# Optimization experiments

Hardware: AMD Instinct MI355X
Metric: run time of the kernel (lower is better)

## Reference

```python
import jax, jax.numpy as jnp
import numpy as np

N_USERS = 100000
N_ITEMS = 100000
N = N_USERS + N_ITEMS
E = 3200000
TXT = 768
GREC = 16
D = 32            # embedding_dim (hardcoded 32 in the torch module)
LAYERS = 3        # len(weight_size)


def setup_inputs() -> dict:
    key = jax.random.key(0)
    ks = jax.random.split(key, 20)
    inp = {}
    inp["edge_row"] = jax.random.randint(ks[0], (E,), 0, N, dtype=jnp.int32)
    inp["edge_col"] = jax.random.randint(ks[1], (E,), 0, N, dtype=jnp.int32)
    # normalized adjacency values (positive, small)
    inp["adj_vals"] = jax.random.uniform(ks[2], (E,), dtype=jnp.float32) * 0.1
    inp["user_name_embs"] = jax.random.normal(ks[3], (N_USERS, TXT), dtype=jnp.float32)
    inp["sent_embs"] = jax.random.normal(ks[4], (N_ITEMS, TXT), dtype=jnp.float32)
    # learned params
    inp["user_emb"] = jax.random.normal(ks[5], (N_USERS, GREC), dtype=jnp.float32) * 0.1
    inp["item_emb"] = jax.random.normal(ks[6], (N_ITEMS, GREC), dtype=jnp.float32) * 0.1
    inp["ue_W1"] = jax.random.normal(ks[7], (TXT, 32), dtype=jnp.float32) * 0.05
    inp["ue_W2"] = jax.random.normal(ks[8], (32, GREC), dtype=jnp.float32) * 0.05
    inp["ie_W1"] = jax.random.normal(ks[9], (TXT, 32), dtype=jnp.float32) * 0.05
    inp["ie_W2"] = jax.random.normal(ks[10], (32, GREC), dtype=jnp.float32) * 0.05
    inp["gc_W"] = jax.random.normal(ks[11], (LAYERS, D, D), dtype=jnp.float32) * 0.1
    inp["gc_b"] = jnp.zeros((LAYERS, D), dtype=jnp.float32)
    inp["bi_W"] = jax.random.normal(ks[12], (LAYERS, D, D), dtype=jnp.float32) * 0.1
    inp["bi_b"] = jnp.zeros((LAYERS, D), dtype=jnp.float32)
    return inp


def _ngcf_forward(edge_row, edge_col, adj_vals, user_name_embs, sent_embs,
                  user_emb, item_emb, ue_W1, ue_W2, ie_W1, ie_W2,
                  gc_W, gc_b, bi_W, bi_b):
    # text encoders (Dropout is identity in eval mode)
    u_created = jax.nn.relu(user_name_embs @ ue_W1) @ ue_W2   # [Nu, 16]
    i_created = jax.nn.relu(sent_embs @ ie_W1) @ ie_W2         # [Ni, 16]
    agg_user = jnp.concatenate([user_emb, u_created], axis=1)  # [Nu, 32]
    agg_item = jnp.concatenate([item_emb, i_created], axis=1)  # [Ni, 32]
    ego = jnp.concatenate([agg_user, agg_item], axis=0)        # [N, 32]

    all_embeddings = [ego]
    for l in range(LAYERS):
        # sparse.mm(adj, ego): gather source rows, scale by edge value, scatter-add
        gathered = adj_vals[:, None] * ego[edge_col]           # [E, 32]
        side = jax.ops.segment_sum(gathered, edge_row, num_segments=N)  # [N, 32]
        sum_emb = jax.nn.leaky_relu(side @ gc_W[l] + gc_b[l])
        bi_emb = jax.nn.leaky_relu((ego * side) @ bi_W[l] + bi_b[l])
        ego = sum_emb + bi_emb                                 # dropout = identity (eval)
        norm = ego / jnp.maximum(
            jnp.linalg.norm(ego, axis=1, keepdims=True), 1e-12)
        all_embeddings.append(norm)
    return jnp.concatenate(all_embeddings, axis=1)             # [N, 32*(LAYERS+1)]


def reference(edge_row, edge_col, adj_vals, user_name_embs, sent_embs,
              user_emb, item_emb, ue_W1, ue_W2, ie_W1, ie_W2,
              gc_W, gc_b, bi_W, bi_b):
    all_e = _ngcf_forward(edge_row, edge_col, adj_vals, user_name_embs, sent_embs,
                          user_emb, item_emb, ue_W1, ue_W2, ie_W1, ie_W2,
                          gc_W, gc_b, bi_W, bi_b)
    u_g = all_e[:N_USERS]
    i_g = all_e[N_USERS:]
    return (u_g, i_g)
```

## Files before the change

kernel.cpp:

```cpp
#include <hip/hip_runtime.h>
#include <cstdint>

#define NU 100000
#define NI 100000
#define NN 200000
#define NE 3200000
#define TXT 768
#define NBF 640

typedef _Float16 f16x8 __attribute__((ext_vector_type(8)));
typedef _Float16 f16x4 __attribute__((ext_vector_type(4)));
typedef float    f32x4 __attribute__((ext_vector_type(4)));

typedef __attribute__((address_space(1))) const unsigned int guint;
typedef __attribute__((address_space(3))) unsigned int luint;

__device__ __forceinline__ float lrelu(float x) { return x >= 0.f ? x : 0.01f * x; }

#define MEMFENCE asm volatile("" ::: "memory")
#define WAIT_VM(N)  asm volatile("s_waitcnt vmcnt(" #N ")" ::: "memory")
#define WAIT_LGKM0  asm volatile("s_waitcnt lgkmcnt(0)" ::: "memory")
#define BARRIER     do { __builtin_amdgcn_s_barrier(); MEMFENCE; } while (0)

__global__ __launch_bounds__(256) void prep_kernel(
    const int* __restrict__ erow,
    const float* __restrict__ uemb, const float* __restrict__ iemb,
    const float* __restrict__ ueW1, const float* __restrict__ ieW1,
    int* __restrict__ cnt,
    _Float16* __restrict__ ego16, float* __restrict__ outp,
    _Float16* __restrict__ w1p)
{
    const int b = blockIdx.x;
    const int tid = threadIdx.x;

    if (b < NBF) {
        const int4* e4 = (const int4*)erow;
        for (int c = b * 256 + tid; c < NE / 4; c += NBF * 256) {
            int4 v = e4[c];
            atomicAdd(&cnt[v.x], 1);
            atomicAdd(&cnt[v.y], 1);
            atomicAdd(&cnt[v.z], 1);
            atomicAdd(&cnt[v.w], 1);
        }
    } else if (b < NBF + 3125) {
        int idx = (b - NBF) * 256 + tid;
        if (idx >= NN * 4) return;
        int n = idx >> 2, q = idx & 3;
        float4 v;
        if (n < NU) v = ((const float4*)uemb)[(size_t)n * 4 + q];
        else        v = ((const float4*)iemb)[(size_t)(n - NU) * 4 + q];
        f16x4 h;
        h[0] = (_Float16)v.x; h[1] = (_Float16)v.y;
        h[2] = (_Float16)v.z; h[3] = (_Float16)v.w;
        *(f16x4*)(ego16 + (size_t)n * 32 + q * 4) = h;
        ((float4*)outp)[(size_t)n * 32 + q] = v;
    } else {
        int i = (b - (NBF + 3125)) * 256 + tid;
        int side = (i >= 24576);
        int ii = i - side * 24576;
        const float* W1 = side ? ieW1 : ueW1;
        int j   = ii & 7;
        int ln  = (ii >> 3) & 63;
        int kbH = ii >> 9;
        int kb  = kbH >> 1, H = kbH & 1;
        int k   = kb * 32 + (ln >> 4) * 8 + j;
        int c   = H * 16 + (ln & 15);
        w1p[i] = (_Float16)W1[k * 32 + c];
    }
}

__global__ __launch_bounds__(256) void scan_blk_kernel(const int* __restrict__ cnt,
                                                       int* __restrict__ rp,
                                                       int* __restrict__ bsum)
{
    __shared__ int ts[256];
    const int tid = threadIdx.x;
    const int base = blockIdx.x * 1024 + tid * 4;
    int v0 = (base + 0 < NN) ? cnt[base + 0] : 0;
    int v1 = (base + 1 < NN) ? cnt[base + 1] : 0;
    int v2 = (base + 2 < NN) ? cnt[base + 2] : 0;
    int v3 = (base + 3 < NN) ? cnt[base + 3] : 0;
    int s = v0 + v1 + v2 + v3;
    ts[tid] = s;
    __syncthreads();
    for (int off = 1; off < 256; off <<= 1) {
        int t = (tid >= off) ? ts[tid - off] : 0;
        __syncthreads();
        ts[tid] += t;
        __syncthreads();
    }
    int excl = ts[tid] - s;
    if (base + 0 < NN) rp[base + 0] = excl;
    if (base + 1 < NN) rp[base + 1] = excl + v0;
    if (base + 2 < NN) rp[base + 2] = excl + v0 + v1;
    if (base + 3 < NN) rp[base + 3] = excl + v0 + v1 + v2;
    if (tid == 255) bsum[blockIdx.x] = ts[255];
}

__global__ __launch_bounds__(256) void scan_bsum_kernel(int* __restrict__ bsum, int nblk)
{
    __shared__ int ts[256];
    const int tid = threadIdx.x;
    int v = (tid < nblk) ? bsum[tid] : 0;
    ts[tid] = v;
    __syncthreads();
    for (int off = 1; off < 256; off <<= 1) {
        int t = (tid >= off) ? ts[tid - off] : 0;
        __syncthreads();
        ts[tid] += t;
        __syncthreads();
    }
    if (tid < nblk) bsum[tid] = ts[tid] - v;
}

__global__ __launch_bounds__(256) void add_off_kernel(int* __restrict__ rp,
                                                      const int* __restrict__ bsum,
                                                      int* __restrict__ cur)
{
    int i = blockIdx.x * 256 + threadIdx.x;
    if (i < NN) {
        int v = rp[i] + bsum[i >> 10];
        rp[i] = v;
        cur[i] = v;
    }
    if (i == 0) rp[NN] = NE;
}

__global__ __launch_bounds__(256, 4) void mlp_fill_kernel(
    const float* __restrict__ Xu, const float* __restrict__ Xi,
    const _Float16* __restrict__ w1pack,
    const float* __restrict__ ueW2, const float* __restrict__ ieW2,
    _Float16* __restrict__ ego16,
    float* __restrict__ outp,
    const int* __restrict__ erow, const int* __restrict__ ecol,
    const float* __restrict__ eval,
    int* __restrict__ cur, uint2* __restrict__ recs)
{
    __shared__ float buf[2][4096];
    __shared__ float part[3][512];
    __shared__ _Float16 hbuf[640];

    const int tid = threadIdx.x;

    if (blockIdx.x >= 1024) {
        const int b = blockIdx.x - 1024;
        const int4*   e4 = (const int4*)erow;
        const int4*   c4 = (const int4*)ecol;
        const float4* f4 = (const float4*)eval;
        for (int c = b * 256 + tid; c < NE / 4; c += NBF * 256) {
            int4 v   = e4[c];
            int4 cc  = c4[c];
            float4 vv = f4[c];
            int p0 = atomicAdd(&cur[v.x], 1);
            recs[p0] = make_uint2((unsigned)cc.x | ((unsigned)(v.x & 63) << 18),
                                  __float_as_uint(vv.x));
            int p1 = atomicAdd(&cur[v.y], 1);
            recs[p1] = make_uint2((unsigned)cc.y | ((unsigned)(v.y & 63) << 18),
                                  __float_as_uint(vv.y));
            int p2 = atomicAdd(&cur[v.z], 1);
            recs[p2] = make_uint2((unsigned)cc.z | ((unsigned)(v.z & 63) << 18),
                                  __float_as_uint(vv.z));
            int p3 = atomicAdd(&cur[v.w], 1);
            recs[p3] = make_uint2((unsigned)cc.w | ((unsigned)(v.w & 63) << 18),
                                  __float_as_uint(vv.w));
        }
        return;
    }

    const int lane  = tid & 63;
    const int wv    = tid >> 6;
    const int row16 = lane & 15;
    const int cg    = lane >> 4;
    const int rx7   = row16 & 7;

    f16x8 bw2u, bw2i;
    #pragma unroll
    for (int j = 0; j < 8; ++j) {
        bw2u[j] = (_Float16)ueW2[((lane >> 4) * 8 + j) * 16 + (lane & 15)];
        bw2i[j] = (_Float16)ieW2[((lane >> 4) * 8 + j) * 16 + (lane & 15)];
    }

    const int tA = (int)(((long)blockIdx.x * 12500) >> 10);
    const int tB = (int)(((long)(blockIdx.x + 1) * 12500) >> 10);

    for (int t = tA; t < tB; ++t) {
        const bool isU = t < 6250;
        const int tile = isU ? t : t - 6250;
        const float* xt = (isU ? Xu : Xi) + (size_t)tile * 16 * TXT;
        const _Float16* w1p = w1pack + (isU ? 0 : 24576);

#define STAGE(bb, cc) do {                                                      \
            _Pragma("unroll")                                                   \
            for (int i_ = 0; i_ < 4; ++i_) {                                    \
                const int r_ = wv * 4 + i_;                                     \
                const float* g_ = xt + (size_t)r_ * TXT + (cc) * 256            \
                                  + ((lane ^ (r_ & 7)) << 2);                   \
                __builtin_amdgcn_global_load_lds((guint*)g_,                    \
                    (luint*)&buf[bb][r_ * 256], 16, 0, 0);                      \
            }                                                                   \
        } while (0)

#define MCHUNK(bb, cc) do {                                                     \
            _Pragma("unroll")                                                   \
            for (int kl2 = 0; kl2 < 2; ++kl2) {                                 \
                const int kbl = wv * 2 + kl2;                                   \
                const int kb  = (cc) * 8 + kbl;                                 \
                f16x8 b0 = *(const f16x8*)&w1p[(kb * 2 + 0) * 512 + lane * 8];  \
                f16x8 b1 = *(const f16x8*)&w1p[(kb * 2 + 1) * 512 + lane * 8];  \
                const int u0 = kbl * 8 + cg * 2;                                \
                f32x4 xa = *(const f32x4*)&buf[bb][row16 * 256 + ((u0 ^ rx7) << 2)]; \
                f32x4 xb = *(const f32x4*)&buf[bb][row16 * 256 + (((u0 + 1) ^ rx7) << 2)]; \
                f16x8 a;                                                        \
                a[0] = (_Float16)xa[0]; a[1] = (_Float16)xa[1];                 \
                a[2] = (_Float16)xa[2]; a[3] = (_Float16)xa[3];                 \
                a[4] = (_Float16)xb[0]; a[5] = (_Float16)xb[1];                 \
                a[6] = (_Float16)xb[2]; a[7] = (_Float16)xb[3];                 \
                c0 = __builtin_amdgcn_mfma_f32_16x16x32_f16(a, b0, c0, 0, 0, 0); \
                c1 = __builtin_amdgcn_mfma_f32_16x16x32_f16(a, b1, c1, 0, 0, 0); \
            }                                                                   \
        } while (0)

        f32x4 c0 = {0.f, 0.f, 0.f, 0.f};
        f32x4 c1 = {0.f, 0.f, 0.f, 0.f};

        STAGE(0, 0);
        STAGE(1, 1);
        WAIT_VM(4);
        BARRIER;
        MCHUNK(0, 0);
        WAIT_LGKM0;
        BARRIER;
        STAGE(0, 2);
        WAIT_VM(4);
        BARRIER;
        MCHUNK(1, 1);
        WAIT_LGKM0;
        WAIT_VM(0);
        BARRIER;
        MCHUNK(0, 2);
        WAIT_LGKM0;

        if (wv > 0) {
            *(f32x4*)&part[wv - 1][lane * 8]     = c0;
            *(f32x4*)&part[wv - 1][lane * 8 + 4] = c1;
            WAIT_LGKM0;
        }
        BARRIER;

        if (wv == 0) {
            #pragma unroll
            for (int p = 0; p < 3; ++p) {
                f32x4 pa = *(const f32x4*)&part[p][lane * 8];
                f32x4 pb = *(const f32x4*)&part[p][lane * 8 + 4];
                c0 += pa; c1 += pb;
            }
            #pragma unroll
            for (int j = 0; j < 4; ++j) {
                int r = cg * 4 + j;
                hbuf[r * 40 + row16]      = (_Float16)fmaxf(c0[j], 0.f);
                hbuf[r * 40 + row16 + 16] = (_Float16)fmaxf(c1[j], 0.f);
            }
            const _Float16* ap = &hbuf[row16 * 40 + cg * 8];
            f16x4 lo = *(const f16x4*)ap;
            f16x4 hi = *(const f16x4*)(ap + 4);
            f16x8 a2;
            a2[0] = lo[0]; a2[1] = lo[1]; a2[2] = lo[2]; a2[3] = lo[3];
            a2[4] = hi[0]; a2[5] = hi[1]; a2[6] = hi[2]; a2[7] = hi[3];

            f32x4 c2 = {0.f, 0.f, 0.f, 0.f};
            f16x8 bw2 = isU ? bw2u : bw2i;
            c2 = __builtin_amdgcn_mfma_f32_16x16x32_f16(a2, bw2, c2, 0, 0, 0);

            const int rbase = (isU ? 0 : NU) + tile * 16 + cg * 4;
            #pragma unroll
            for (int j = 0; j < 4; ++j) {
                float v = c2[j];
                ego16[(size_t)(rbase + j) * 32  + 16 + row16] = (_Float16)v;
                outp [(size_t)(rbase + j) * 128 + 16 + row16] = v;
            }
        }
#undef STAGE
#undef MCHUNK
    }
}

__global__ __launch_bounds__(256) void pull_update_v2(
    const int* __restrict__ rp, const uint2* __restrict__ recs,
    const _Float16* __restrict__ egoIn, _Float16* __restrict__ egoOut,
    float* __restrict__ outp,
    const float* __restrict__ gcW, const float* __restrict__ gcb,
    const float* __restrict__ biW, const float* __restrict__ bib, int l)
{
    __shared__ float acc[64][33];
    __shared__ float Wg[32][36];
    __shared__ float Wb[32][36];
    __shared__ float bgs[32], bbs[32];

    const int tid = threadIdx.x;
    for (int i = tid; i < 64 * 33; i += 256) ((float*)acc)[i] = 0.f;
    for (int i = tid; i < 1024; i += 256) {
        Wg[i >> 5][i & 31] = gcW[l * 1024 + i];
        Wb[i >> 5][i & 31] = biW[l * 1024 + i];
    }
    if (tid < 32) { bgs[tid] = gcb[l * 32 + tid]; bbs[tid] = bib[l * 32 + tid]; }

    const int r0 = blockIdx.x * 64;
    const int eBeg = rp[r0], eEnd = rp[r0 + 64];
    __syncthreads();

    const int cnt = eEnd - eBeg;
    const int s   = tid >> 3;
    const int q   = tid & 7;
    const int L   = (cnt + 31) >> 5;
    const int e0  = eBeg + s * L;
    const int e1  = min(e0 + L, eEnd);

    float4 a4 = make_float4(0.f, 0.f, 0.f, 0.f);
    int curRl = -1;

    auto PROC = [&](uint2 rr, f16x4 vv) {
        int rl = rr.x >> 18;
        float a = __uint_as_float(rr.y);
        if (rl != curRl) {
            if (curRl >= 0) {
                atomicAdd(&acc[curRl][q * 4 + 0], a4.x);
                atomicAdd(&acc[curRl][q * 4 + 1], a4.y);
                atomicAdd(&acc[curRl][q * 4 + 2], a4.z);
                atomicAdd(&acc[curRl][q * 4 + 3], a4.w);
            }
            a4 = make_float4(0.f, 0.f, 0.f, 0.f);
            curRl = rl;
        }
        a4.x += a * (float)vv[0];
        a4.y += a * (float)vv[1];
        a4.z += a * (float)vv[2];
        a4.w += a * (float)vv[3];
    };

    int e = e0;
    for (; e + 8 <= e1; e += 8) {
        uint2 r0r = recs[e],     r1r = recs[e + 1];
        uint2 r2r = recs[e + 2], r3r = recs[e + 3];
        uint2 r4r = recs[e + 4], r5r = recs[e + 5];
        uint2 r6r = recs[e + 6], r7r = recs[e + 7];
        f16x4 v0 = *(const f16x4*)(egoIn + (size_t)(r0r.x & 0x3FFFF) * 32 + q * 4);
        f16x4 v1 = *(const f16x4*)(egoIn + (size_t)(r1r.x & 0x3FFFF) * 32 + q * 4);
        f16x4 v2 = *(const f16x4*)(egoIn + (size_t)(r2r.x & 0x3FFFF) * 32 + q * 4);
        f16x4 v3 = *(const f16x4*)(egoIn + (size_t)(r3r.x & 0x3FFFF) * 32 + q * 4);
        f16x4 v4 = *(const f16x4*)(egoIn + (size_t)(r4r.x & 0x3FFFF) * 32 + q * 4);
        f16x4 v5 = *(const f16x4*)(egoIn + (size_t)(r5r.x & 0x3FFFF) * 32 + q * 4);
        f16x4 v6 = *(const f16x4*)(egoIn + (size_t)(r6r.x & 0x3FFFF) * 32 + q * 4);
        f16x4 v7 = *(const f16x4*)(egoIn + (size_t)(r7r.x & 0x3FFFF) * 32 + q * 4);
        PROC(r0r, v0); PROC(r1r, v1); PROC(r2r, v2); PROC(r3r, v3);
        PROC(r4r, v4); PROC(r5r, v5); PROC(r6r, v6); PROC(r7r, v7);
    }
    for (; e < e1; ++e) {
        uint2 rr = recs[e];
        f16x4 vv = *(const f16x4*)(egoIn + (size_t)(rr.x & 0x3FFFF) * 32 + q * 4);
        PROC(rr, vv);
    }
    if (curRl >= 0) {
        atomicAdd(&acc[curRl][q * 4 + 0], a4.x);
        atomicAdd(&acc[curRl][q * 4 + 1], a4.y);
        atomicAdd(&acc[curRl][q * 4 + 2], a4.z);
        atomicAdd(&acc[curRl][q * 4 + 3], a4.w);
    }
    __syncthreads();

    const int r    = tid >> 2;
    const int c    = tid & 3;
    const int node = r0 + r;
    const int j0   = c * 8;

    const _Float16* er = egoIn + (size_t)node * 32;
    f16x8 ev0 = *(const f16x8*)er;
    f16x8 ev1 = *(const f16x8*)(er + 8);
    f16x8 ev2 = *(const f16x8*)(er + 16);
    f16x8 ev3 = *(const f16x8*)(er + 24);

    float A[8], B[8];
    #pragma unroll
    for (int jj = 0; jj < 8; ++jj) { A[jj] = bgs[j0 + jj]; B[jj] = bbs[j0 + jj]; }

    #pragma unroll
    for (int kq = 0; kq < 4; ++kq) {
        #pragma unroll
        for (int kk = 0; kk < 8; ++kk) {
            const int k = kq * 8 + kk;
            float sk = acc[r][k];
            float evk = (kq == 0) ? (float)ev0[kk] : (kq == 1) ? (float)ev1[kk]
                      : (kq == 2) ? (float)ev2[kk] : (float)ev3[kk];
            float ek = sk * evk;
            f32x4 g0 = *(const f32x4*)&Wg[k][j0];
            f32x4 g1 = *(const f32x4*)&Wg[k][j0 + 4];
            f32x4 b0 = *(const f32x4*)&Wb[k][j0];
            f32x4 b1 = *(const f32x4*)&Wb[k][j0 + 4];
            A[0] += sk * g0[0]; A[1] += sk * g0[1]; A[2] += sk * g0[2]; A[3] += sk * g0[3];
            A[4] += sk * g1[0]; A[5] += sk * g1[1]; A[6] += sk * g1[2]; A[7] += sk * g1[3];
            B[0] += ek * b0[0]; B[1] += ek * b0[1]; B[2] += ek * b0[2]; B[3] += ek * b0[3];
            B[4] += ek * b1[0]; B[5] += ek * b1[1]; B[6] += ek * b1[2]; B[7] += ek * b1[3];
        }
    }

    float v[8];
    float ss = 0.f;
    #pragma unroll
    for (int jj = 0; jj < 8; ++jj) {
        float x = lrelu(A[jj]) + lrelu(B[jj]);
        v[jj] = x;
        ss += x * x;
    }
    ss += __shfl_xor(ss, 1, 64);
    ss += __shfl_xor(ss, 2, 64);
    float inv = 1.0f / fmaxf(sqrtf(ss), 1e-12f);

    f16x8 h;
    #pragma unroll
    for (int jj = 0; jj < 8; ++jj) h[jj] = (_Float16)v[jj];
    *(f16x8*)(egoOut + (size_t)node * 32 + j0) = h;

    float* op = outp + (size_t)node * 128 + (size_t)(l + 1) * 32 + j0;
    float4 o0 = make_float4(v[0] * inv, v[1] * inv, v[2] * inv, v[3] * inv);
    float4 o1 = make_float4(v[4] * inv, v[5] * inv, v[6] * inv, v[7] * inv);
    *(float4*)op       = o0;
    *(float4*)(op + 4) = o1;
}

extern "C" void kernel_launch(void* const* d_in, const int* in_sizes, int n_in,
                              void* d_out, int out_size, void* d_ws, size_t ws_size,
                              hipStream_t stream)
{
    const int*   erow = (const int*)d_in[0];
    const int*   ecol = (const int*)d_in[1];
    const float* evalp = (const float*)d_in[2];
    const float* une  = (const float*)d_in[3];
    const float* se   = (const float*)d_in[4];
    const float* uemb = (const float*)d_in[5];
    const float* iemb = (const float*)d_in[6];
    const float* ueW1 = (const float*)d_in[7];
    const float* ueW2 = (const float*)d_in[8];
    const float* ieW1 = (const float*)d_in[9];
    const float* ieW2 = (const float*)d_in[10];
    const float* gcW  = (const float*)d_in[11];
    const float* gcb  = (const float*)d_in[12];
    const float* biW  = (const float*)d_in[13];
    const float* bib  = (const float*)d_in[14];
    float* outp = (float*)d_out;

    _Float16* egoA16 = (_Float16*)d_ws;
    _Float16* egoB16 = egoA16 + (size_t)NN * 32;
    uint2* recs = (uint2*)(egoB16 + (size_t)NN * 32);
    int*   cnt  = (int*)(recs + (size_t)NE);
    int*   rp   = cnt + NN;
    int*   cur  = rp + NN + 1;
    int*   bsum = cur + NN;
    _Float16* w1pack = (_Float16*)(bsum + 256);

    const size_t need = (size_t)((char*)(w1pack + 49152) - (char*)d_ws);
    if (ws_size < need) return;

    hipMemsetAsync(cnt, 0, (size_t)NN * sizeof(int), stream);
    prep_kernel<<<NBF + 3125 + 192, 256, 0, stream>>>(erow, uemb, iemb, ueW1, ieW1,
                                                      cnt, egoA16, outp, w1pack);

    const int NBLK = (NN + 1023) / 1024;
    scan_blk_kernel<<<NBLK, 256, 0, stream>>>(cnt, rp, bsum);
    scan_bsum_kernel<<<1, 256, 0, stream>>>(bsum, NBLK);
    add_off_kernel<<<(NN + 255) / 256, 256, 0, stream>>>(rp, bsum, cur);

    mlp_fill_kernel<<<1024 + NBF, 256, 0, stream>>>(
        une, se, w1pack, ueW2, ieW2, egoA16, outp,
        erow, ecol, evalp, cur, recs);

    const _Float16* egoIn = egoA16;
    _Float16* egoOut = egoB16;
    for (int l = 0; l < 3; ++l) {
        pull_update_v2<<<NN / 64, 256, 0, stream>>>(rp, recs, egoIn, egoOut, outp,
                                                    gcW, gcb, biW, bib, l);
        const _Float16* t = egoOut; egoOut = (_Float16*)egoIn; egoIn = t;
    }
}
```

Baseline: 666.4 us.

## Halve MLP staging chunk size to raise occupancy in mlp_fill_kernel

The text-encoder MLP now stages input in 128-float chunks instead of 256, so each 16-row tile takes six pipeline stages instead of three. The LDS staging buffer shrinks by half and the launch-bounds hint rises from 4 to 6 blocks per SM. The aim is more resident blocks to hide global-load latency. In exchange there are more barriers and wait points per tile, and each wave issues only one MFMA pair per chunk.

```diff
diff --git a/kernel.cpp b/kernel.cpp
--- a/kernel.cpp
+++ b/kernel.cpp
@@ -126,7 +126,7 @@
     if (i == 0) rp[NN] = NE;
 }
 
-__global__ __launch_bounds__(256, 4) void mlp_fill_kernel(
+__global__ __launch_bounds__(256, 6) void mlp_fill_kernel(
     const float* __restrict__ Xu, const float* __restrict__ Xi,
     const _Float16* __restrict__ w1pack,
     const float* __restrict__ ueW2, const float* __restrict__ ieW2,
@@ -136,7 +136,7 @@
     const float* __restrict__ eval,
     int* __restrict__ cur, uint2* __restrict__ recs)
 {
-    __shared__ float buf[2][4096];
+    __shared__ float buf[2][2048];
     __shared__ float part[3][512];
     __shared__ _Float16 hbuf[640];
 
@@ -191,54 +191,54 @@
 
 #define STAGE(bb, cc) do {                                                      \
             _Pragma("unroll")                                                   \
-            for (int i_ = 0; i_ < 4; ++i_) {                                    \
-                const int r_ = wv * 4 + i_;                                     \
-                const float* g_ = xt + (size_t)r_ * TXT + (cc) * 256            \
-                                  + ((lane ^ (r_ & 7)) << 2);                   \
+            for (int i_ = 0; i_ < 2; ++i_) {                                    \
+                const int rb_ = wv * 4 + i_ * 2;                                \
+                const int r_  = rb_ + (lane >> 5);                              \
+                const float* g_ = xt + (size_t)r_ * TXT + (cc) * 128            \
+                                  + (((lane & 31) ^ (r_ & 7)) << 2);            \
                 __builtin_amdgcn_global_load_lds((guint*)g_,                    \
-                    (luint*)&buf[bb][r_ * 256], 16, 0, 0);                      \
+                    (luint*)&buf[bb][rb_ * 128], 16, 0, 0);                     \
             }                                                                   \
         } while (0)
 
 #define MCHUNK(bb, cc) do {                                                     \
-            _Pragma("unroll")                                                   \
-            for (int kl2 = 0; kl2 < 2; ++kl2) {                                 \
-                const int kbl = wv * 2 + kl2;                                   \
-                const int kb  = (cc) * 8 + kbl;                                 \
-                f16x8 b0 = *(const f16x8*)&w1p[(kb * 2 + 0) * 512 + lane * 8];  \
-                f16x8 b1 = *(const f16x8*)&w1p[(kb * 2 + 1) * 512 + lane * 8];  \
-                const int u0 = kbl * 8 + cg * 2;                                \
-                f32x4 xa = *(const f32x4*)&buf[bb][row16 * 256 + ((u0 ^ rx7) << 2)]; \
-                f32x4 xb = *(const f32x4*)&buf[bb][row16 * 256 + (((u0 + 1) ^ rx7) << 2)]; \
-                f16x8 a;                                                        \
-                a[0] = (_Float16)xa[0]; a[1] = (_Float16)xa[1];                 \
-                a[2] = (_Float16)xa[2]; a[3] = (_Float16)xa[3];                 \
-                a[4] = (_Float16)xb[0]; a[5] = (_Float16)xb[1];                 \
-                a[6] = (_Float16)xb[2]; a[7] = (_Float16)xb[3];                 \
-                c0 = __builtin_amdgcn_mfma_f32_16x16x32_f16(a, b0, c0, 0, 0, 0); \
-                c1 = __builtin_amdgcn_mfma_f32_16x16x32_f16(a, b1, c1, 0, 0, 0); \
-            }                                                                   \
+            const int kb = (cc) * 4 + wv;                                       \
+            f16x8 b0 = *(const f16x8*)&w1p[(kb * 2 + 0) * 512 + lane * 8];      \
+            f16x8 b1 = *(const f16x8*)&w1p[(kb * 2 + 1) * 512 + lane * 8];      \
+            const int u0 = wv * 8 + cg * 2;                                     \
+            f32x4 xa = *(const f32x4*)&buf[bb][row16 * 128 + ((u0 ^ rx7) << 2)]; \
+            f32x4 xb = *(const f32x4*)&buf[bb][row16 * 128 + (((u0 + 1) ^ rx7) << 2)]; \
+            f16x8 a;                                                            \
+            a[0] = (_Float16)xa[0]; a[1] = (_Float16)xa[1];                     \
+            a[2] = (_Float16)xa[2]; a[3] = (_Float16)xa[3];                     \
+            a[4] = (_Float16)xb[0]; a[5] = (_Float16)xb[1];                     \
+            a[6] = (_Float16)xb[2]; a[7] = (_Float16)xb[3];                     \
+            c0 = __builtin_amdgcn_mfma_f32_16x16x32_f16(a, b0, c0, 0, 0, 0);    \
+            c1 = __builtin_amdgcn_mfma_f32_16x16x32_f16(a, b1, c1, 0, 0, 0);    \
         } while (0)
 
         f32x4 c0 = {0.f, 0.f, 0.f, 0.f};
         f32x4 c1 = {0.f, 0.f, 0.f, 0.f};
 
+
         STAGE(0, 0);
         STAGE(1, 1);
-        WAIT_VM(4);
-        BARRIER;
-        MCHUNK(0, 0);
-        WAIT_LGKM0;
-        BARRIER;
+        WAIT_VM(2);  BARRIER;
+        MCHUNK(0, 0); WAIT_LGKM0; BARRIER;
         STAGE(0, 2);
-        WAIT_VM(4);
-        BARRIER;
-        MCHUNK(1, 1);
-        WAIT_LGKM0;
-        WAIT_VM(0);
-        BARRIER;
-        MCHUNK(0, 2);
-        WAIT_LGKM0;
+        WAIT_VM(2);  BARRIER;
+        MCHUNK(1, 1); WAIT_LGKM0; BARRIER;
+        STAGE(1, 3);
+        WAIT_VM(2);  BARRIER;
+        MCHUNK(0, 2); WAIT_LGKM0; BARRIER;
+        STAGE(0, 4);
+        WAIT_VM(2);  BARRIER;
+        MCHUNK(1, 3); WAIT_LGKM0; BARRIER;
+        STAGE(1, 5);
+        WAIT_VM(2);  BARRIER;
+        MCHUNK(0, 4); WAIT_LGKM0;
+        WAIT_VM(0);  BARRIER;
+        MCHUNK(1, 5); WAIT_LGKM0;
 
         if (wv > 0) {
             *(f32x4*)&part[wv - 1][lane * 8]     = c0;
```

After: 635.5 us. -4.6%, faster.
